# Kernel optimization log

Measured on AMD Instinct MI355X. Metric: run time of the kernel, lower is better.

## Reference

```python
import jax, jax.numpy as jnp
import numpy as np

EMBED_DIM = 64       # embedding_dim (latent channels)
NUM_ATOMS = 1024     # num_embeddings (dictionary atoms)
SPARSITY = 8         # sparsity_level
N_PIXELS = 16384     # flattened latent pixels (e.g. B=16, 32x32 grid)
DIAG_EPS = 1e-4
CHOL_EPS = 1e-6


def setup_inputs() -> dict:
    key = jax.random.key(0)
    kx, kd = jax.random.split(key)
    X = jax.random.normal(kx, (EMBED_DIM, N_PIXELS), dtype=jnp.float32)
    # dictionary parameter initialized as randn * 0.02, per the module __init__
    D = jax.random.normal(kd, (EMBED_DIM, NUM_ATOMS), dtype=jnp.float32) * 0.02
    return {"X": X, "D": D}


def _nan0(x):
    return jnp.nan_to_num(x, nan=0.0, posinf=0.0, neginf=0.0)


def _batched_omp(X, D, sparsity_level):
    """Batched OMP with sequential Cholesky updates.

    X: [d, N] signals, D: [d, K] dictionary.
    Returns (I [N, S] int32 support indices, coeffs [N, S] ordered coefficients).
    """
    X = _nan0(X)
    D = _nan0(D)
    d, n = X.shape
    k = D.shape[1]
    rows = jnp.arange(n)

    G = D.T @ D + DIAG_EPS * jnp.eye(k, dtype=D.dtype)   # [K, K] Gram
    h_bar = (D.T @ X).T                                   # [N, K] correlations
    h = h_bar
    mask = jnp.zeros((n, k), dtype=bool)                  # selected-atom mask
    L = None                                              # batched Cholesky [N, s, s]
    I = jnp.zeros((n, 0), dtype=jnp.int32)
    coeffs = jnp.zeros((n, 0), dtype=X.dtype)

    for s in range(sparsity_level):  # static unroll, S is small
        scores = jnp.where(mask, jnp.asarray(-1.0, X.dtype), jnp.abs(h))
        idx = jnp.argmax(scores, axis=1)                  # [N]
        mask = mask.at[rows, idx].set(True)
        diag_g = G[idx, idx][:, None, None]               # [N, 1, 1]
        if s == 0:
            L = jnp.sqrt(jnp.clip(diag_g, CHOL_EPS))      # [N, 1, 1]
        else:
            # G[I[n, j], idx[n]] for each batch element n -> [N, s, 1]
            G_col = G[I, idx[:, None]][..., None]
            w = jax.scipy.linalg.solve_triangular(L, G_col, lower=True)  # [N, s, 1]
            wt = jnp.swapaxes(w, 1, 2)                                   # [N, 1, s]
            corner = jnp.sqrt(jnp.clip(diag_g - jnp.sum(w * w, axis=1, keepdims=True), CHOL_EPS))
            zeros_col = jnp.zeros((n, s, 1), dtype=X.dtype)
            L = jnp.concatenate(
                [jnp.concatenate([L, zeros_col], axis=2),
                 jnp.concatenate([wt, corner], axis=2)], axis=1)          # [N, s+1, s+1]
        I = jnp.concatenate([I, idx[:, None].astype(jnp.int32)], axis=1)  # [N, s+1]
        # solve (L L^T) x = h_bar[support] via two triangular solves (cholesky_solve)
        h_stack = jnp.take_along_axis(h_bar, I, axis=1)[..., None]        # [N, s+1, 1]
        y = jax.scipy.linalg.solve_triangular(L, h_stack, lower=True)
        x_stack = jax.scipy.linalg.solve_triangular(jnp.swapaxes(L, 1, 2), y, lower=False)
        coeffs = _nan0(x_stack[..., 0])                                   # [N, s+1]
        # beta = coeffs @ G[support, :]  -> residual correlation update
        beta = jnp.einsum('ns,nsk->nk', coeffs, G[I])
        h = _nan0(h_bar - beta)
    return I, coeffs


def reference(X, D):
    I, coeffs = _batched_omp(X, D, SPARSITY)
    atoms = D[:, I]                                  # [d, N, S]
    recon = jnp.einsum('ns,dns->nd', coeffs, atoms)  # [N, d] sparse reconstruction
    return recon, I, coeffs
```

## Files before the change

### kernel.cpp

```cpp
#include <hip/hip_runtime.h>
#include <cmath>

#define NPIX 16384
#define NATOM 1024
#define DIM 64
#define SPAR 8

__global__ __launch_bounds__(256) void k_pre(const float* __restrict__ X,
                                             const float* __restrict__ D,
                                             float* __restrict__ G,
                                             float* __restrict__ Dt,
                                             float* __restrict__ Gd,
                                             float* __restrict__ HB) {
  __shared__ float smem[2 * DIM * 128];
  const int b = blockIdx.x;
  if (b < 256) {
    const int i0 = (b >> 4) * 64, j0 = (b & 15) * 64;
    float(*sA)[65] = (float(*)[65])smem;
    float(*sB)[65] = (float(*)[65])(smem + DIM * 65);
    for (int t = threadIdx.x; t < DIM * 16; t += 256) {
      int d = t >> 4, c4 = (t & 15) * 4;
      *reinterpret_cast<float4*>(&sA[d][c4]) =
          *reinterpret_cast<const float4*>(&D[(size_t)d * NATOM + i0 + c4]);
      *reinterpret_cast<float4*>(&sB[d][c4]) =
          *reinterpret_cast<const float4*>(&D[(size_t)d * NATOM + j0 + c4]);
    }
    __syncthreads();
    const int ty = (threadIdx.x >> 4) * 4;
    const int tx = (threadIdx.x & 15) * 4;
    double acc[4][4];
#pragma unroll
    for (int ii = 0; ii < 4; ++ii)
#pragma unroll
      for (int jj = 0; jj < 4; ++jj) acc[ii][jj] = 0.0;
    for (int d = 0; d < DIM; ++d) {
      float a[4], bb[4];
#pragma unroll
      for (int ii = 0; ii < 4; ++ii) a[ii] = sA[d][ty + ii];
#pragma unroll
      for (int jj = 0; jj < 4; ++jj) bb[jj] = sB[d][tx + jj];
#pragma unroll
      for (int ii = 0; ii < 4; ++ii)
#pragma unroll
        for (int jj = 0; jj < 4; ++jj)
          acc[ii][jj] += (double)a[ii] * (double)bb[jj];
    }
#pragma unroll
    for (int ii = 0; ii < 4; ++ii)
#pragma unroll
      for (int jj = 0; jj < 4; ++jj) {
        const int k1 = i0 + ty + ii, k2 = j0 + tx + jj;
        float g = (float)acc[ii][jj];
        if (k1 == k2) {
          g += 1e-4f;
          Gd[k1] = g;
        }
        G[(size_t)k1 * NATOM + k2] = g;
      }
  } else if (b < 320) {
    const int base = (b - 256) * 1024 + threadIdx.x * 4;
    float4 v = *reinterpret_cast<const float4*>(&D[base]);
    const float vv[4] = {v.x, v.y, v.z, v.w};
#pragma unroll
    for (int e = 0; e < 4; ++e) {
      int idx = base + e;
      Dt[(size_t)(idx & (NATOM - 1)) * DIM + (idx >> 10)] = vv[e];
    }
  } else {
    const int bx = b - 320;
    const int n0 = (bx & 127) * 128, k0 = (bx >> 7) * 128;
    float(*sX)[128] = (float(*)[128])smem;
    float(*sD)[128] = (float(*)[128])(smem + DIM * 128);
    for (int i = threadIdx.x; i < DIM * 32; i += 256) {
      int d = i >> 5, c4 = (i & 31) * 4;
      *reinterpret_cast<float4*>(&sX[d][c4]) =
          *reinterpret_cast<const float4*>(&X[(size_t)d * NPIX + n0 + c4]);
      *reinterpret_cast<float4*>(&sD[d][c4]) =
          *reinterpret_cast<const float4*>(&D[(size_t)d * NATOM + k0 + c4]);
    }
    __syncthreads();
    const int nl = (threadIdx.x & 15) * 8;
    const int kl = (threadIdx.x >> 4) * 8;
    float acc[8][8];
#pragma unroll
    for (int i = 0; i < 8; ++i)
#pragma unroll
      for (int j = 0; j < 8; ++j) acc[i][j] = 0.f;
#pragma unroll 4
    for (int d = 0; d < DIM; ++d) {
      float xv[8], dv[8];
      *reinterpret_cast<float4*>(&xv[0]) = *reinterpret_cast<float4*>(&sX[d][nl]);
      *reinterpret_cast<float4*>(&xv[4]) = *reinterpret_cast<float4*>(&sX[d][nl + 4]);
      *reinterpret_cast<float4*>(&dv[0]) = *reinterpret_cast<float4*>(&sD[d][kl]);
      *reinterpret_cast<float4*>(&dv[4]) = *reinterpret_cast<float4*>(&sD[d][kl + 4]);
#pragma unroll
      for (int i = 0; i < 8; ++i)
#pragma unroll
        for (int j = 0; j < 8; ++j) acc[i][j] = fmaf(xv[i], dv[j], acc[i][j]);
    }
#pragma unroll
    for (int i = 0; i < 8; ++i)
#pragma unroll
      for (int j = 0; j < 2; ++j)
        *reinterpret_cast<float4*>(
            &HB[(size_t)(n0 + nl + i) * NATOM + k0 + kl + j * 4]) =
            *reinterpret_cast<float4*>(&acc[i][j * 4]);
  }
}

template <int CTRL>
__device__ __forceinline__ float dpp_fmax(float x) {
  int s = __builtin_amdgcn_update_dpp(__float_as_int(x), __float_as_int(x),
                                      CTRL, 0xf, 0xf, false);
  return fmaxf(x, __int_as_float(s));
}
__device__ __forceinline__ float wave_max_bcast(float x) {
  x = dpp_fmax<0x111>(x);
  x = dpp_fmax<0x112>(x);
  x = dpp_fmax<0x114>(x);
  x = dpp_fmax<0x118>(x);
  x = dpp_fmax<0x142>(x);
  x = dpp_fmax<0x143>(x);
  return __int_as_float(__builtin_amdgcn_readlane(__float_as_int(x), 63));
}

template <bool HBWS, bool DTW>
__global__ __launch_bounds__(64) void k_omp(const float* __restrict__ HB,
                                            const float* __restrict__ X,
                                            const float* __restrict__ D,
                                            const float* __restrict__ Dt,
                                            const float* __restrict__ G,
                                            const float* __restrict__ Gd,
                                            float* __restrict__ out) {
  const int lane = threadIdx.x & 63;
  const int lane16 = lane * 16;
  const int n = __builtin_amdgcn_readfirstlane(blockIdx.x);

  float hb[16];
  if (HBWS) {
#pragma unroll
    for (int q = 0; q < 4; ++q) {
      float4 v = *reinterpret_cast<const float4*>(
          &HB[(size_t)n * NATOM + lane16 + q * 4]);
      hb[q * 4 + 0] = v.x; hb[q * 4 + 1] = v.y;
      hb[q * 4 + 2] = v.z; hb[q * 4 + 3] = v.w;
    }
  } else {
    double a[16];
#pragma unroll
    for (int j = 0; j < 16; ++j) a[j] = 0.0;
    for (int d = 0; d < DIM; ++d) {
      float xd = X[(size_t)d * NPIX + n];
#pragma unroll
      for (int j = 0; j < 16; ++j)
        a[j] += (double)xd * (double)D[(size_t)d * NATOM + lane16 + j];
    }
#pragma unroll
    for (int j = 0; j < 16; ++j) hb[j] = (float)a[j];
  }
#pragma unroll
  for (int j = 0; j < 16; ++j) asm volatile("" : "+v"(hb[j]));

  int selI[SPAR];
  float rows[SPAR - 1][16];
  float Lm[SPAR][SPAR], invL[SPAR], ysel[SPAR], coefF[SPAR];

#pragma unroll 8
  for (int s = 0; s < SPAR; ++s) {
    float h[16];
#pragma unroll
    for (int j = 0; j < 16; ++j) {
      float hv = hb[j];
#pragma unroll
      for (int i = 0; i < SPAR - 1; ++i)
        if (i < s) hv = fmaf(-coefF[i], rows[i][j], hv);
      h[j] = hv;
    }
    float m0 = fmaxf(fmaxf(fmaxf(fabsf(h[0]), fabsf(h[1])), fabsf(h[2])), fabsf(h[3]));
    float m1 = fmaxf(fmaxf(fmaxf(fabsf(h[4]), fabsf(h[5])), fabsf(h[6])), fabsf(h[7]));
    float m2 = fmaxf(fmaxf(fmaxf(fabsf(h[8]), fabsf(h[9])), fabsf(h[10])), fabsf(h[11]));
    float m3 = fmaxf(fmaxf(fmaxf(fabsf(h[12]), fabsf(h[13])), fabsf(h[14])), fabsf(h[15]));
    const float M = wave_max_bcast(fmaxf(fmaxf(m0, m1), fmaxf(m2, m3)));
    unsigned cand = NATOM;
#pragma unroll
    for (int j = 15; j >= 0; --j)
      cand = (fabsf(h[j]) == M) ? (unsigned)(lane16 + j) : cand;
    unsigned long long bal = __ballot(cand != (unsigned)NATOM);
    const int fl = __ffsll(bal) - 1;
    const int bk = __builtin_amdgcn_readlane((int)cand, fl);
    selI[s] = bk;
    const int bl = bk >> 4, bj = bk & 15;

    float hbs;
    if (HBWS) {
      hbs = HB[(size_t)n * NATOM + bk];
    } else {
      float v = 0.f;
#pragma unroll
      for (int j = 0; j < 16; ++j)
        if (j == bj) v = hb[j];
      hbs = __int_as_float(__builtin_amdgcn_readlane(__float_as_int(v), bl));
    }

#pragma unroll
    for (int j = 0; j < 16; ++j)
      if (j == bj && lane == bl) hb[j] = __builtin_nanf("");

    if (s < SPAR - 1) {
#pragma unroll
      for (int q = 0; q < 4; ++q) {
        float4 rv = *reinterpret_cast<const float4*>(
            &G[(size_t)bk * NATOM + lane16 + q * 4]);
        rows[s][q * 4 + 0] = rv.x; rows[s][q * 4 + 1] = rv.y;
        rows[s][q * 4 + 2] = rv.z; rows[s][q * 4 + 3] = rv.w;
      }
    }

    const float diag = Gd[bk];
    float w[SPAR];
    float sq = 0.f;
#pragma unroll
    for (int i = 0; i < SPAR; ++i)
      if (i < s) {
        float a = G[(size_t)selI[i] * NATOM + bk];
#pragma unroll
        for (int t = 0; t < SPAR; ++t)
          if (t < i) a = fmaf(-Lm[i][t], w[t], a);
        w[i] = a * invL[i];
        sq += w[i] * w[i];
        Lm[s][i] = w[i];
      }
    float cc = diag - sq;
    if (cc < 1e-6f) cc = 1e-6f;
    invL[s] = 1.0f / sqrtf(cc);

    {
      float a = hbs;
#pragma unroll
      for (int t = 0; t < SPAR; ++t)
        if (t < s) a = fmaf(-Lm[s][t], ysel[t], a);
      ysel[s] = a * invL[s];
    }
#pragma unroll
    for (int i = SPAR - 1; i >= 0; --i)
      if (i <= s) {
        float a = ysel[i];
#pragma unroll
        for (int t = 0; t < SPAR; ++t)
          if (t > i && t <= s) a = fmaf(-Lm[t][i], coefF[t], a);
        coefF[i] = a * invL[i];
      }

    if (s < SPAR - 1) {
#pragma unroll
      for (int j = 0; j < 16; ++j) asm volatile("" : "+v"(rows[s][j]));
    }
  }

  double r = 0.0;
#pragma unroll
  for (int i = 0; i < SPAR; ++i) {
    float dv = DTW ? Dt[(size_t)selI[i] * DIM + lane]
                   : D[(size_t)lane * NATOM + selI[i]];
    r += (double)coefF[i] * (double)dv;
  }
  out[(size_t)n * DIM + lane] = (float)r;

  float fi = 0.f, fc = 0.f;
#pragma unroll
  for (int i = 0; i < SPAR; ++i)
    if (lane == i) { fi = (float)selI[i]; fc = coefF[i]; }
  if (lane < SPAR) {
    out[(size_t)NPIX * DIM + (size_t)n * SPAR + lane] = fi;
    out[(size_t)NPIX * DIM + (size_t)NPIX * SPAR + (size_t)n * SPAR + lane] = fc;
  }
}

__global__ __launch_bounds__(256) void k_gram(const float* __restrict__ D,
                                              float* __restrict__ G,
                                              float* __restrict__ Gd) {
  int k1 = blockIdx.x;
  __shared__ float d1[DIM];
  if (threadIdx.x < DIM) d1[threadIdx.x] = D[(size_t)threadIdx.x * NATOM + k1];
  __syncthreads();
  for (int k2 = threadIdx.x; k2 < NATOM; k2 += 256) {
    double acc = 0.0;
#pragma unroll
    for (int d = 0; d < DIM; ++d)
      acc += (double)d1[d] * (double)D[(size_t)d * NATOM + k2];
    float g = (float)acc;
    if (k2 == k1) {
      g += 1e-4f;
      Gd[k1] = g;
    }
    G[(size_t)k1 * NATOM + k2] = g;
  }
}

extern "C" void kernel_launch(void* const* d_in, const int* in_sizes, int n_in,
                              void* d_out, int out_size, void* d_ws,
                              size_t ws_size, hipStream_t stream) {
  const float* X = (const float*)d_in[0];
  const float* D = (const float*)d_in[1];
  float* out = (float*)d_out;
  float* G = (float*)d_ws;
  float* Dt = G + (size_t)NATOM * NATOM;
  float* Gd = Dt + (size_t)NATOM * DIM;
  float* HB = Gd + NATOM;
  const size_t needFull =
      ((size_t)NATOM * NATOM + (size_t)NATOM * DIM + NATOM +
       (size_t)NPIX * NATOM) * sizeof(float);

  if (ws_size >= needFull) {
    k_pre<<<dim3(1344), dim3(256), 0, stream>>>(X, D, G, Dt, Gd, HB);
    k_omp<true, true><<<dim3(NPIX), dim3(64), 0, stream>>>(
        HB, X, D, Dt, G, Gd, out);
  } else {
    k_gram<<<dim3(NATOM), dim3(256), 0, stream>>>(D, G, Gd);
    k_omp<false, false><<<dim3(NPIX), dim3(64), 0, stream>>>(
        nullptr, X, D, nullptr, G, Gd, out);
  }
}
```

Before: 110.1 us.

## Split each pixel's OMP across two waves with shared-memory argmax merge

The main OMP kernel now gives each pixel two 64-lane waves, each owning 512 atoms with 8 values per lane, instead of one wave holding 16 per lane. Per-wave argmax results go through a small double-buffered shared array and one __syncthreads per step, then both waves redundantly run the small Cholesky update. The aim is to halve per-thread register state and the per-step correlation update, raising occupancy and parallelism. The cost is a block barrier per iteration and duplicated scalar Cholesky work in both waves. The fallback path is split out into its own non-templated kernel.

```diff
diff --git a/kernel.cpp b/kernel.cpp
--- a/kernel.cpp
+++ b/kernel.cpp
@@ -124,28 +124,157 @@
   return __int_as_float(__builtin_amdgcn_readlane(__float_as_int(x), 63));
 }
 
-template <bool HBWS, bool DTW>
-__global__ __launch_bounds__(64) void k_omp(const float* __restrict__ HB,
-                                            const float* __restrict__ X,
-                                            const float* __restrict__ D,
-                                            const float* __restrict__ Dt,
-                                            const float* __restrict__ G,
-                                            const float* __restrict__ Gd,
-                                            float* __restrict__ out) {
+__global__ __launch_bounds__(128, 3) void k_omp2(const float* __restrict__ HB,
+                                                 const float* __restrict__ Dt,
+                                                 const float* __restrict__ G,
+                                                 const float* __restrict__ Gd,
+                                                 float* __restrict__ out) {
+  const int lane = threadIdx.x & 63;
+  const int wave = threadIdx.x >> 6;
+  const int kbase = wave * 512 + lane * 8;
+  const int n = __builtin_amdgcn_readfirstlane(blockIdx.x);
+
+  __shared__ float sM[2][2];
+  __shared__ int sC[2][2];
+
+  float hb[8];
+#pragma unroll
+  for (int q = 0; q < 2; ++q) {
+    float4 v = *reinterpret_cast<const float4*>(
+        &HB[(size_t)n * NATOM + kbase + q * 4]);
+    hb[q * 4 + 0] = v.x; hb[q * 4 + 1] = v.y;
+    hb[q * 4 + 2] = v.z; hb[q * 4 + 3] = v.w;
+  }
+#pragma unroll
+  for (int j = 0; j < 8; ++j) asm volatile("" : "+v"(hb[j]));
+
+  int selI[SPAR];
+  float rows[SPAR - 1][8];
+  float Lm[SPAR][SPAR], invL[SPAR], ysel[SPAR], coefF[SPAR];
+
+#pragma unroll 8
+  for (int s = 0; s < SPAR; ++s) {
+    float h[8];
+#pragma unroll
+    for (int j = 0; j < 8; ++j) {
+      float hv = hb[j];
+#pragma unroll
+      for (int i = 0; i < SPAR - 1; ++i)
+        if (i < s) hv = fmaf(-coefF[i], rows[i][j], hv);
+      h[j] = hv;
+    }
+    float ml = fmaxf(fmaxf(fmaxf(fabsf(h[0]), fabsf(h[1])), fabsf(h[2])), fabsf(h[3]));
+    float mh = fmaxf(fmaxf(fmaxf(fabsf(h[4]), fabsf(h[5])), fabsf(h[6])), fabsf(h[7]));
+    const float Mw = wave_max_bcast(fmaxf(ml, mh));
+    unsigned cand = NATOM;
+#pragma unroll
+    for (int j = 7; j >= 0; --j)
+      cand = (fabsf(h[j]) == Mw) ? (unsigned)(kbase + j) : cand;
+    unsigned long long bal = __ballot(cand != (unsigned)NATOM);
+    const int fl = __ffsll(bal) - 1;
+    const int cw = __builtin_amdgcn_readlane((int)cand, fl);
+    if (lane == 0) {
+      sM[s & 1][wave] = Mw;
+      sC[s & 1][wave] = cw;
+    }
+    __syncthreads();
+    const float M0 = sM[s & 1][0], M1 = sM[s & 1][1];
+    const int c0 = sC[s & 1][0], c1 = sC[s & 1][1];
+    int bkv;
+    if (M0 > M1) bkv = c0;
+    else if (M1 > M0) bkv = c1;
+    else bkv = c0 < c1 ? c0 : c1;
+    const int bk = __builtin_amdgcn_readfirstlane(bkv);
+    selI[s] = bk;
+
+    const float hbs = HB[(size_t)n * NATOM + bk];
+
+    if ((bk >> 9) == wave && lane == ((bk >> 3) & 63)) {
+#pragma unroll
+      for (int j = 0; j < 8; ++j)
+        if (j == (bk & 7)) hb[j] = __builtin_nanf("");
+    }
+
+    if (s < SPAR - 1) {
+#pragma unroll
+      for (int q = 0; q < 2; ++q) {
+        float4 rv = *reinterpret_cast<const float4*>(
+            &G[(size_t)bk * NATOM + kbase + q * 4]);
+        rows[s][q * 4 + 0] = rv.x; rows[s][q * 4 + 1] = rv.y;
+        rows[s][q * 4 + 2] = rv.z; rows[s][q * 4 + 3] = rv.w;
+      }
+    }
+
+    const float diag = Gd[bk];
+    float w[SPAR];
+    float sq = 0.f;
+#pragma unroll
+    for (int i = 0; i < SPAR; ++i)
+      if (i < s) {
+        float a = G[(size_t)selI[i] * NATOM + bk];
+#pragma unroll
+        for (int t = 0; t < SPAR; ++t)
+          if (t < i) a = fmaf(-Lm[i][t], w[t], a);
+        w[i] = a * invL[i];
+        sq += w[i] * w[i];
+        Lm[s][i] = w[i];
+      }
+    float cc = diag - sq;
+    if (cc < 1e-6f) cc = 1e-6f;
+    invL[s] = 1.0f / sqrtf(cc);
+
+    {
+      float a = hbs;
+#pragma unroll
+      for (int t = 0; t < SPAR; ++t)
+        if (t < s) a = fmaf(-Lm[s][t], ysel[t], a);
+      ysel[s] = a * invL[s];
+    }
+#pragma unroll
+    for (int i = SPAR - 1; i >= 0; --i)
+      if (i <= s) {
+        float a = ysel[i];
+#pragma unroll
+        for (int t = 0; t < SPAR; ++t)
+          if (t > i && t <= s) a = fmaf(-Lm[t][i], coefF[t], a);
+        coefF[i] = a * invL[i];
+      }
+
+    if (s < SPAR - 1) {
+#pragma unroll
+      for (int j = 0; j < 8; ++j) asm volatile("" : "+v"(rows[s][j]));
+    }
+  }
+
+  if (wave == 0) {
+    double r = 0.0;
+#pragma unroll
+    for (int i = 0; i < SPAR; ++i)
+      r += (double)coefF[i] * (double)Dt[(size_t)selI[i] * DIM + lane];
+    out[(size_t)n * DIM + lane] = (float)r;
+  } else {
+    float fi = 0.f, fc = 0.f;
+#pragma unroll
+    for (int i = 0; i < SPAR; ++i)
+      if (lane == i) { fi = (float)selI[i]; fc = coefF[i]; }
+    if (lane < SPAR) {
+      out[(size_t)NPIX * DIM + (size_t)n * SPAR + lane] = fi;
+      out[(size_t)NPIX * DIM + (size_t)NPIX * SPAR + (size_t)n * SPAR + lane] = fc;
+    }
+  }
+}
+
+__global__ __launch_bounds__(64) void k_omp_fb(const float* __restrict__ X,
+                                               const float* __restrict__ D,
+                                               const float* __restrict__ G,
+                                               const float* __restrict__ Gd,
+                                               float* __restrict__ out) {
   const int lane = threadIdx.x & 63;
   const int lane16 = lane * 16;
   const int n = __builtin_amdgcn_readfirstlane(blockIdx.x);
 
   float hb[16];
-  if (HBWS) {
-#pragma unroll
-    for (int q = 0; q < 4; ++q) {
-      float4 v = *reinterpret_cast<const float4*>(
-          &HB[(size_t)n * NATOM + lane16 + q * 4]);
-      hb[q * 4 + 0] = v.x; hb[q * 4 + 1] = v.y;
-      hb[q * 4 + 2] = v.z; hb[q * 4 + 3] = v.w;
-    }
-  } else {
+  {
     double a[16];
 #pragma unroll
     for (int j = 0; j < 16; ++j) a[j] = 0.0;
@@ -191,16 +320,12 @@
     selI[s] = bk;
     const int bl = bk >> 4, bj = bk & 15;
 
-    float hbs;
-    if (HBWS) {
-      hbs = HB[(size_t)n * NATOM + bk];
-    } else {
-      float v = 0.f;
-#pragma unroll
-      for (int j = 0; j < 16; ++j)
-        if (j == bj) v = hb[j];
-      hbs = __int_as_float(__builtin_amdgcn_readlane(__float_as_int(v), bl));
-    }
+    float v = 0.f;
+#pragma unroll
+    for (int j = 0; j < 16; ++j)
+      if (j == bj) v = hb[j];
+    const float hbs =
+        __int_as_float(__builtin_amdgcn_readlane(__float_as_int(v), bl));
 
 #pragma unroll
     for (int j = 0; j < 16; ++j)
@@ -233,7 +358,6 @@
     float cc = diag - sq;
     if (cc < 1e-6f) cc = 1e-6f;
     invL[s] = 1.0f / sqrtf(cc);
-
     {
       float a = hbs;
 #pragma unroll
@@ -250,7 +374,6 @@
           if (t > i && t <= s) a = fmaf(-Lm[t][i], coefF[t], a);
         coefF[i] = a * invL[i];
       }
-
     if (s < SPAR - 1) {
 #pragma unroll
       for (int j = 0; j < 16; ++j) asm volatile("" : "+v"(rows[s][j]));
@@ -259,11 +382,8 @@
 
   double r = 0.0;
 #pragma unroll
-  for (int i = 0; i < SPAR; ++i) {
-    float dv = DTW ? Dt[(size_t)selI[i] * DIM + lane]
-                   : D[(size_t)lane * NATOM + selI[i]];
-    r += (double)coefF[i] * (double)dv;
-  }
+  for (int i = 0; i < SPAR; ++i)
+    r += (double)coefF[i] * (double)D[(size_t)lane * NATOM + selI[i]];
   out[(size_t)n * DIM + lane] = (float)r;
 
   float fi = 0.f, fc = 0.f;
@@ -313,11 +433,9 @@
 
   if (ws_size >= needFull) {
     k_pre<<<dim3(1344), dim3(256), 0, stream>>>(X, D, G, Dt, Gd, HB);
-    k_omp<true, true><<<dim3(NPIX), dim3(64), 0, stream>>>(
-        HB, X, D, Dt, G, Gd, out);
+    k_omp2<<<dim3(NPIX), dim3(128), 0, stream>>>(HB, Dt, G, Gd, out);
   } else {
     k_gram<<<dim3(NATOM), dim3(256), 0, stream>>>(D, G, Gd);
-    k_omp<false, false><<<dim3(NPIX), dim3(64), 0, stream>>>(
-        nullptr, X, D, nullptr, G, Gd, out);
-  }
-}
+    k_omp_fb<<<dim3(NPIX), dim3(64), 0, stream>>>(X, D, G, Gd, out);
+  }
+}
```

Measured after the change: 112.7 us. 1.02x slower.
